# Optimization experiments

Hardware: AMD Instinct MI355X
Metric: run time of the kernel (lower is better)

## Reference

```python
import jax, jax.numpy as jnp
import numpy as np

HEADS = 16
HIDDEN = 1024
D_HEAD = HIDDEN // HEADS
SCALE = float(D_HEAD) ** 0.5


def setup_inputs() -> dict:
    key = jax.random.key(0)
    ks = jax.random.split(key, 11)
    B, L = 2, 2048
    x = jax.random.normal(ks[0], (B, L, HIDDEN), dtype=jnp.float32)
    # 0/1 padding mask, broadcast over heads and query positions
    mask = jax.random.randint(ks[1], (B, 1, 1, L), 0, 2).astype(jnp.float32)
    s = 1.0 / np.sqrt(HIDDEN)
    Wq = jax.random.normal(ks[2], (HIDDEN, HIDDEN), dtype=jnp.float32) * s
    bq = jax.random.normal(ks[3], (HIDDEN,), dtype=jnp.float32) * s
    Wk = jax.random.normal(ks[4], (HIDDEN, HIDDEN), dtype=jnp.float32) * s
    bk = jax.random.normal(ks[5], (HIDDEN,), dtype=jnp.float32) * s
    Wv = jax.random.normal(ks[6], (HIDDEN, HIDDEN), dtype=jnp.float32) * s
    bv = jax.random.normal(ks[7], (HIDDEN,), dtype=jnp.float32) * s
    Wo = jax.random.normal(ks[8], (HIDDEN, HIDDEN), dtype=jnp.float32) * s
    bo = jax.random.normal(ks[9], (HIDDEN,), dtype=jnp.float32) * s
    return {"x": x, "mask": mask, "Wq": Wq, "bq": bq, "Wk": Wk, "bk": bk,
            "Wv": Wv, "bv": bv, "Wo": Wo, "bo": bo}


def reference(x, mask, Wq, bq, Wk, bk, Wv, bv, Wo, bo):
    B, L, _ = x.shape
    # projections (Linear: x @ W + b), split heads -> [B, H, L, Dh]
    def proj(W, b):
        return (jnp.dot(x, W) + b).reshape(B, L, HEADS, D_HEAD).transpose(0, 2, 1, 3)
    q = proj(Wq, bq)
    k = proj(Wk, bk)
    v = proj(Wv, bv)
    # scaled dot-product with additive mask: scores [B, H, Lq, Lk]
    scores = jnp.einsum('bhqd,bhkd->bhqk', q, k) / SCALE + mask * (-10000.0)
    attn = jax.nn.softmax(scores, axis=-1)  # dropout p=0.0 -> identity
    out = jnp.einsum('bhqk,bhkd->bhqd', attn, v)
    out = out.transpose(0, 2, 1, 3).reshape(B, L, HIDDEN)
    return jnp.dot(out, Wo) + bo
```

## Files before the change

### kernel.cpp

```cpp
#include <hip/hip_runtime.h>
#include <math.h>

typedef unsigned short u16;
typedef short v8s __attribute__((ext_vector_type(8)));
typedef float v4f __attribute__((ext_vector_type(4)));
typedef float v16f __attribute__((ext_vector_type(16)));

#define HIDDEN 1024
#define L_SEQ 2048
#define NH 16
#define DH 64
#define NKMAX 1280

#define QSCALE 0.18033688011112042f

__device__ __forceinline__ u16 f2bf(float f) {
  union { float f; unsigned int i; } c; c.f = f;
  unsigned int x = c.i;
  unsigned int r = (x + 0x7fffu + ((x >> 16) & 1u)) >> 16;
  return (u16)r;
}

#if defined(__has_builtin)
#if __has_builtin(__builtin_amdgcn_cvt_pk_bf16_f32)
#define HAS_PKBF 1
#endif
#if __has_builtin(__builtin_amdgcn_exp2f)
#define EXP2(x) __builtin_amdgcn_exp2f(x)
#endif
#if __has_builtin(__builtin_amdgcn_rcpf)
#define RCP(x) __builtin_amdgcn_rcpf(x)
#endif
#endif
#ifndef EXP2
#define EXP2(x) exp2f(x)
#endif
#ifndef RCP
#define RCP(x) (1.0f / (x))
#endif

__device__ __forceinline__ unsigned pkbf(float a, float b) {
#ifdef HAS_PKBF
  typedef __bf16 v2bf __attribute__((ext_vector_type(2)));
  union { v2bf v; unsigned u; } c;
  c.v = __builtin_amdgcn_cvt_pk_bf16_f32(a, b);
  return c.u;
#else
  return (unsigned)f2bf(a) | ((unsigned)f2bf(b) << 16);
#endif
}

__device__ __forceinline__ void gload16(const void* g, void* l) {
  void* gg = const_cast<void*>(g);
  __builtin_amdgcn_global_load_lds(
      (__attribute__((address_space(1))) void*)gg,
      (__attribute__((address_space(3))) void*)l, 16, 0, 0);
}

__device__ __forceinline__ v16f vzero16() {
  v16f z;
#pragma unroll
  for (int i = 0; i < 16; ++i) z[i] = 0.f;
  return z;
}

__global__ __launch_bounds__(256) void prep(
    const float* __restrict__ x, u16* __restrict__ xb,
    const float* __restrict__ Wq, const float* __restrict__ Wk,
    const float* __restrict__ Wv, const float* __restrict__ Wo,
    u16* __restrict__ WtQ, u16* __restrict__ WtK,
    u16* __restrict__ WtV, u16* __restrict__ WtO,
    const float* __restrict__ maskg, u16* __restrict__ keep,
    unsigned* __restrict__ nkslot) {
  const int bid = blockIdx.x;
  const int t = threadIdx.x;

  if (bid < 2048) {
    const int i = (bid * 256 + t) * 8;
    const float4 a = *(const float4*)(x + i);
    const float4 b = *(const float4*)(x + i + 4);
    unsigned o[4] = {pkbf(a.x, a.y), pkbf(a.z, a.w), pkbf(b.x, b.y), pkbf(b.z, b.w)};
    *(uint4*)(xb + i) = *(const uint4*)o;
    return;
  }

  if (bid < 6144) {
    const int m = bid - 2048;
    const int z = m >> 10;
    const int rem = m & 1023;
    const int bx = rem & 31, by = rem >> 5;
    const float* src; u16* dst;
    if (z == 0) { src = Wq; dst = WtQ; }
    else if (z == 1) { src = Wk; dst = WtK; }
    else if (z == 2) { src = Wv; dst = WtV; }
    else { src = Wo; dst = WtO; }

    __shared__ u16 tile[32][33];
    const int tx = t & 31, ty = t >> 5;
    const int xcol = bx * 32 + tx;
    const int y0 = by * 32;
#pragma unroll
    for (int i = ty; i < 32; i += 8)
      tile[i][tx] = f2bf(src[(size_t)(y0 + i) * HIDDEN + xcol]);
    __syncthreads();
    const int xo = y0 + tx;
#pragma unroll
    for (int i = ty; i < 32; i += 8)
      dst[(size_t)(bx * 32 + i) * HIDDEN + xo] = tile[tx][i];
    return;
  }

  if (t < 64) {
    const int b = bid - 6144;
    const int lane = t;
    const float* mp = maskg + b * L_SEQ;
    int cnt = 0;
#pragma unroll 1
    for (int j = 0; j < 32; ++j) cnt += (mp[lane * 32 + j] == 0.0f) ? 1 : 0;
    int inc = cnt;
#pragma unroll
    for (int off = 1; off < 64; off <<= 1) {
      const int v = __shfl_up(inc, off, 64);
      if (lane >= off) inc += v;
    }
    int base = inc - cnt;
    u16* kp = keep + b * L_SEQ;
#pragma unroll 1
    for (int j = 0; j < 32; ++j) {
      const int k = lane * 32 + j;
      if (mp[k] == 0.0f) kp[base++] = (u16)k;
    }
    const int total = __shfl(inc, 63, 64);
    for (int i = total + lane; i < NKMAX; i += 64) kp[i] = 0;
    if (lane == 0) nkslot[b] = (unsigned)total;
  }
}

__global__ __launch_bounds__(256) void gemm128(
    const u16* __restrict__ A,
    const u16* __restrict__ B0, const u16* __restrict__ B1, const u16* __restrict__ B2,
    const float* __restrict__ bias0, const float* __restrict__ bias1, const float* __restrict__ bias2,
    u16* __restrict__ C0, u16* __restrict__ C1, u16* __restrict__ C2,
    float* __restrict__ Cf, const u16* __restrict__ keep,
    const unsigned* __restrict__ nkslot,
    int qkv_mode) {
  __shared__ __align__(16) u16 As[128 * 32];
  __shared__ __align__(16) u16 Bs[128 * 32];

  const u16* Bt; const float* bias; u16* C;
  if (blockIdx.z == 0) { Bt = B0; bias = bias0; C = C0; }
  else if (blockIdx.z == 1) { Bt = B1; bias = bias1; C = C1; }
  else { Bt = B2; bias = bias2; C = C2; }
  const int mode = qkv_mode ? (blockIdx.z == 0 ? 1 : (blockIdx.z == 1 ? 2 : 3)) : 0;
  const float oscale = (mode == 1) ? QSCALE : 1.0f;

  const int t = threadIdx.x;
  const int lane = t & 63;
  const int wave = t >> 6;
  const int quad = lane >> 4;
  const int l16 = lane & 15;
  const int wm = wave >> 1;
  const int wn = wave & 1;

  const int n0 = blockIdx.x * 128;
  const int sr = t >> 2;
  const int sc = (t & 3) * 8;

  int m0 = blockIdx.y * 128;
  int kvb = 0;
  const u16* Ag0;
  const u16* Ag1;
  if (mode == 2 || mode == 3) {
    const int y = blockIdx.y;
    if (y >= 20) return;
    kvb = y / 10;
    m0 = (y % 10) * 128;
    const unsigned nk = nkslot[kvb];
    if ((unsigned)m0 >= ((nk + 63u) & ~63u)) return;
    const int sr0 = keep[kvb * L_SEQ + m0 + sr];
    const int sr1 = keep[kvb * L_SEQ + m0 + 64 + sr];
    Ag0 = A + ((size_t)(kvb * L_SEQ + sr0)) * HIDDEN + sc;
    Ag1 = A + ((size_t)(kvb * L_SEQ + sr1)) * HIDDEN + sc;
  } else {
    Ag0 = A + (size_t)(m0 + sr) * HIDDEN + sc;
    Ag1 = Ag0 + (size_t)64 * HIDDEN;
  }
  const u16* Bg0 = Bt + (size_t)(n0 + sr) * HIDDEN + sc;
  const u16* Bg1 = Bg0 + (size_t)64 * HIDDEN;
  u16* Al0 = &As[sr * 32 + sc];
  u16* Al1 = &As[(64 + sr) * 32 + sc];
  u16* Bl0 = &Bs[sr * 32 + sc];
  u16* Bl1 = &Bs[(64 + sr) * 32 + sc];

  v4f acc[4][4];
#pragma unroll
  for (int mi = 0; mi < 4; ++mi)
#pragma unroll
    for (int ni = 0; ni < 4; ++ni)
      acc[mi][ni] = (v4f){0.f, 0.f, 0.f, 0.f};

  for (int k0 = 0; k0 < HIDDEN; k0 += 32) {
    __syncthreads();
    gload16(Ag0 + k0, Al0);
    gload16(Ag1 + k0, Al1);
    gload16(Bg0 + k0, Bl0);
    gload16(Bg1 + k0, Bl1);
    __syncthreads();

    v8s a[4], b[4];
#pragma unroll
    for (int mi = 0; mi < 4; ++mi)
      a[mi] = *(const v8s*)&As[(wm * 64 + mi * 16 + l16) * 32 + quad * 8];
#pragma unroll
    for (int ni = 0; ni < 4; ++ni)
      b[ni] = *(const v8s*)&Bs[(wn * 64 + ni * 16 + l16) * 32 + quad * 8];
#pragma unroll
    for (int mi = 0; mi < 4; ++mi)
#pragma unroll
      for (int ni = 0; ni < 4; ++ni)
        acc[mi][ni] = __builtin_amdgcn_mfma_f32_16x16x32_bf16(a[mi], b[ni], acc[mi][ni], 0, 0, 0);
  }

#pragma unroll
  for (int ni = 0; ni < 4; ++ni) {
    const int col = n0 + wn * 64 + ni * 16 + l16;
    const float bv = bias[col];
#pragma unroll
    for (int mi = 0; mi < 4; ++mi) {
      const int row0 = m0 + wm * 64 + mi * 16 + quad * 4;
      const float v0 = (acc[mi][ni][0] + bv) * oscale;
      const float v1 = (acc[mi][ni][1] + bv) * oscale;
      const float v2 = (acc[mi][ni][2] + bv) * oscale;
      const float v3 = (acc[mi][ni][3] + bv) * oscale;
      if (mode == 0) {
        Cf[(size_t)(row0 + 0) * HIDDEN + col] = v0;
        Cf[(size_t)(row0 + 1) * HIDDEN + col] = v1;
        Cf[(size_t)(row0 + 2) * HIDDEN + col] = v2;
        Cf[(size_t)(row0 + 3) * HIDDEN + col] = v3;
      } else if (mode == 1) {
        const int hh = col >> 6, d = col & 63;
        const float vv[4] = {v0, v1, v2, v3};
#pragma unroll
        for (int i = 0; i < 4; ++i) {
          const int rr = row0 + i;
          const int bb = rr >> 11, l = rr & 2047;
          C[((size_t)(bb * NH + hh) * L_SEQ + l) * DH + d] = f2bf(vv[i]);
        }
      } else if (mode == 2) {
        const int hh = col >> 6, d = col & 63;
        const float vv[4] = {v0, v1, v2, v3};
#pragma unroll
        for (int i = 0; i < 4; ++i)
          C[((size_t)(kvb * NH + hh) * L_SEQ + row0 + i) * DH + d] = f2bf(vv[i]);
      } else {
        const int hh = col >> 6, d = col & 63;
        unsigned pk[2] = {pkbf(v0, v1), pkbf(v2, v3)};
        *(uint2*)&C[((size_t)((kvb * NH + hh) * DH + d)) * L_SEQ + row0] = *(const uint2*)pk;
      }
    }
  }
}


#define XCH(D0_, D2_, A_, B_)                                        \
  {                                                                  \
    unsigned a_ = (A_), b_ = (B_);                                   \
    asm("v_permlane32_swap_b32 %0, %1" : "+v"(a_), "+v"(b_));        \
    D0_ = a_;                                      \
    D2_ = b_;                                      \
  }

#define MKPF(dst, P0, P1, P2, P3, P4, P5, P6, P7)                    \
  {                                                                  \
    const unsigned A_ = pkbf(P0, P1), C_ = pkbf(P2, P3);             \
    const unsigned B_ = pkbf(P4, P5), D_ = pkbf(P6, P7);             \
    union { unsigned u[4]; v8s v; } f_;                              \
    XCH(f_.u[0], f_.u[2], A_, B_);                                   \
    XCH(f_.u[1], f_.u[3], C_, D_);                                   \
    dst = f_.v;                                                      \
  }

__global__ __launch_bounds__(512) void attn512(
    const u16* __restrict__ Qg, const u16* __restrict__ Kcg, const u16* __restrict__ VTg,
    const unsigned* __restrict__ nkslot, u16* __restrict__ Og) {
  __shared__ __align__(16) u16 lds[32768];

  const int t = threadIdx.x;
  const int lane = t & 63;
  const int w = t >> 6;
  const int l31 = lane & 31;
  const int hi = lane >> 5;
  const int e7 = l31 & 7;

  const int bid = blockIdx.x;
  const int bh = bid & 31;
  const int q0 = (bid >> 5) * 256;
  const int b = bh >> 4;
  const int h = bh & 15;

  const size_t base = (size_t)bh * L_SEQ * DH;
  const u16* Qp = Qg + base;
  const u16* Kp = Kcg + base;
  const u16* VTp = VTg + base;

  const int nkb = (int)nkslot[b];
  const int ntiles = (nkb + 127) >> 7;

  const int r8 = lane >> 3, sl8 = lane & 7;
  const int koff = (w * 8 + r8) * DH + (sl8 ^ r8) * 8;
  const int r4 = lane >> 4, sl16 = lane & 15;
  const int vrow = w * 4 + r4;
  const int voff = vrow * L_SEQ + ((((sl16 & 7) ^ (vrow & 7)) | (sl16 & 8)) * 8);
  u16* const kd = &lds[(w * 8) * 64];
  u16* const vd = &lds[16384 + (w * 4) * 128];

  gload16(Kp + koff, kd);
  gload16(Kp + 64 * DH + koff, kd + 64 * 64);
  gload16(VTp + voff, vd);
  gload16(VTp + 32 * L_SEQ + voff, vd + 32 * 128);

  const int qrow = q0 + w * 32 + l31;
  v8s qf[4];
#pragma unroll
  for (int dc = 0; dc < 4; ++dc)
    qf[dc] = *(const v8s*)&Qp[(size_t)qrow * DH + dc * 16 + hi * 8];

  v16f oacc0 = vzero16(), oacc1 = vzero16();
  float lsum = 0.f;

  for (int n = 0; n < ntiles; ++n) {
    __syncthreads();
    const int ksb = (n & 1) * 8192;
    const int vtb = 16384 + (n & 1) * 8192;
    if (n + 1 < ntiles) {
      const size_t k1 = (size_t)(n + 1) * 128;
      const int s2 = ((n + 1) & 1) * 8192;
      gload16(Kp + k1 * DH + koff, kd + s2);
      gload16(Kp + (k1 + 64) * DH + koff, kd + s2 + 64 * 64);
      gload16(VTp + k1 + voff, vd + s2);
      gload16(VTp + k1 + 32 * L_SEQ + voff, vd + s2 + 32 * 128);
    }

    const int kb0 = n * 128;
#pragma unroll
    for (int hh = 0; hh < 2; ++hh) {
      const int h2 = hh ^ (w >> 2);
      v16f s0 = vzero16(), s1 = vzero16();
      __builtin_amdgcn_s_setprio(1);
#pragma unroll
      for (int dc = 0; dc < 4; ++dc) {
        const int po = ((dc * 2 + hi) ^ e7) * 8;
        const v8s kf0 = *(const v8s*)&lds[ksb + (h2 * 64 + l31) * 64 + po];
        const v8s kf1 = *(const v8s*)&lds[ksb + (h2 * 64 + 32 + l31) * 64 + po];
        s0 = __builtin_amdgcn_mfma_f32_32x32x16_bf16(kf0, qf[dc], s0, 0, 0, 0);
        s1 = __builtin_amdgcn_mfma_f32_32x32x16_bf16(kf1, qf[dc], s1, 0, 0, 0);
      }
      __builtin_amdgcn_s_setprio(0);

      const int kh0 = kb0 + h2 * 64;
      float p[32];
#pragma unroll
      for (int r = 0; r < 16; ++r) {
        p[r]      = EXP2(s0[r]);
        p[16 + r] = EXP2(s1[r]);
      }
      if (kh0 + 64 > nkb) {
#pragma unroll
        for (int r = 0; r < 16; ++r) {
          const int kk = kh0 + (r & 3) + 8 * (r >> 2) + 4 * hi;
          if (kk >= nkb) p[r] = 0.f;
          if (kk + 32 >= nkb) p[16 + r] = 0.f;
        }
      }
      {
        float a0 = 0.f, a1 = 0.f, a2 = 0.f, a3 = 0.f;
#pragma unroll
        for (int r = 0; r < 8; ++r) {
          a0 += p[r]; a1 += p[8 + r]; a2 += p[16 + r]; a3 += p[24 + r];
        }
        lsum += (a0 + a1) + (a2 + a3);
      }

      v8s pf0, pf1, pf2, pf3;
      MKPF(pf0, p[0],  p[1],  p[2],  p[3],  p[4],  p[5],  p[6],  p[7]);
      MKPF(pf1, p[8],  p[9],  p[10], p[11], p[12], p[13], p[14], p[15]);
      MKPF(pf2, p[16], p[17], p[18], p[19], p[20], p[21], p[22], p[23]);
      MKPF(pf3, p[24], p[25], p[26], p[27], p[28], p[29], p[30], p[31]);

      __builtin_amdgcn_s_setprio(1);
#pragma unroll
      for (int kc = 0; kc < 4; ++kc) {
        const v8s pb = (kc == 0) ? pf0 : (kc == 1) ? pf1 : (kc == 2) ? pf2 : pf3;
        const int oc = h2 * 8 + kc * 2 + hi;
        const int po = (((oc & 7) ^ e7) | (oc & 8)) * 8;
        const v8s vf0 = *(const v8s*)&lds[vtb + l31 * 128 + po];
        const v8s vf1 = *(const v8s*)&lds[vtb + (32 + l31) * 128 + po];
        oacc0 = __builtin_amdgcn_mfma_f32_32x32x16_bf16(vf0, pb, oacc0, 0, 0, 0);
        oacc1 = __builtin_amdgcn_mfma_f32_32x32x16_bf16(vf1, pb, oacc1, 0, 0, 0);
      }
      __builtin_amdgcn_s_setprio(0);
    }
  }

  const float ltot = lsum + __shfl(lsum, lane ^ 32, 64);
  const float linv = RCP(ltot);

  const size_t ob = ((size_t)(b * L_SEQ + qrow)) * HIDDEN + h * DH;
#pragma unroll
  for (int r = 0; r < 16; r += 2) {
    const int d0 = (r & 3) + 8 * (r >> 2) + 4 * hi;
    const unsigned w0 = pkbf(oacc0[r] * linv, oacc0[r + 1] * linv);
    const unsigned w1 = pkbf(oacc1[r] * linv, oacc1[r + 1] * linv);
    *(unsigned*)&Og[ob + d0] = w0;
    *(unsigned*)&Og[ob + 32 + d0] = w1;
  }
}

extern "C" void kernel_launch(void* const* d_in, const int* in_sizes, int n_in,
                              void* d_out, int out_size, void* d_ws, size_t ws_size,
                              hipStream_t stream) {
  const float* x    = (const float*)d_in[0];
  const float* mask = (const float*)d_in[1];
  const float* Wq   = (const float*)d_in[2];
  const float* bq   = (const float*)d_in[3];
  const float* Wk   = (const float*)d_in[4];
  const float* bk   = (const float*)d_in[5];
  const float* Wv   = (const float*)d_in[6];
  const float* bv   = (const float*)d_in[7];
  const float* Wo   = (const float*)d_in[8];
  const float* bo   = (const float*)d_in[9];
  float* out = (float*)d_out;
  u16* ws = (u16*)d_ws;

  const unsigned M1 = 1u << 20;
  u16* WtQ = ws;
  u16* WtK = ws + M1;
  u16* WtV = ws + 2 * M1;
  u16* WtO = ws + 3 * M1;
  u16* xb  = ws + 4 * M1;
  u16* Qb  = ws + 8 * M1;
  u16* Kc  = ws + 12 * M1;
  u16* VTc = ws + 16 * M1;
  u16* Ob  = ws + 20 * M1;
  u16* keep = ws + 16 * M1 - 8192;
  unsigned* nkslot = (unsigned*)(ws + 16 * M1 - 8192 - 8);

  prep<<<6146, 256, 0, stream>>>(x, xb, Wq, Wk, Wv, Wo, WtQ, WtK, WtV, WtO,
                                 mask, keep, nkslot);
  gemm128<<<dim3(8, 32, 3), 256, 0, stream>>>(xb, WtQ, WtK, WtV, bq, bk, bv,
                                              Qb, Kc, VTc, nullptr, keep, nkslot, 1);
  attn512<<<dim3(256), 512, 0, stream>>>(Qb, Kc, VTc, nkslot, Ob);
  gemm128<<<dim3(8, 32, 1), 256, 0, stream>>>(Ob, WtO, WtO, WtO, bo, bo, bo,
                                              nullptr, nullptr, nullptr, out, nullptr, nullptr, 0);
}
```

Before: 183.9 us.

## Deepen GEMM K-tile to 64 with XOR-swizzled LDS and XCD-aware block mapping

The projection GEMM now stages a 64-wide K slice per iteration instead of 32, which halves the number of barrier pairs and global-load rounds. The LDS layout is XOR-swizzled by row so the wider rows do not cause bank conflicts on the fragment reads. Launches switch to a 1D grid that is remapped so each XCD gets a contiguous band of M rows, aiming for better L2 reuse of A and B tiles. LDS use per block doubles, which may lower occupancy.

```diff
diff --git a/kernel.cpp b/kernel.cpp
--- a/kernel.cpp
+++ b/kernel.cpp
@@ -144,14 +144,22 @@
     float* __restrict__ Cf, const u16* __restrict__ keep,
     const unsigned* __restrict__ nkslot,
     int qkv_mode) {
-  __shared__ __align__(16) u16 As[128 * 32];
-  __shared__ __align__(16) u16 Bs[128 * 32];
+  __shared__ __align__(16) u16 As[128 * 64];
+  __shared__ __align__(16) u16 Bs[128 * 64];
+
+  const int wgid = blockIdx.x;
+  const int xcd = wgid & 7;
+  const int j = wgid >> 3;
+  const int bx = j & 7;
+  const int rem = j >> 3;
+  const int by = xcd * 4 + (rem & 3);
+  const int bz = rem >> 2;
 
   const u16* Bt; const float* bias; u16* C;
-  if (blockIdx.z == 0) { Bt = B0; bias = bias0; C = C0; }
-  else if (blockIdx.z == 1) { Bt = B1; bias = bias1; C = C1; }
+  if (bz == 0) { Bt = B0; bias = bias0; C = C0; }
+  else if (bz == 1) { Bt = B1; bias = bias1; C = C1; }
   else { Bt = B2; bias = bias2; C = C2; }
-  const int mode = qkv_mode ? (blockIdx.z == 0 ? 1 : (blockIdx.z == 1 ? 2 : 3)) : 0;
+  const int mode = qkv_mode ? (bz == 0 ? 1 : (bz == 1 ? 2 : 3)) : 0;
   const float oscale = (mode == 1) ? QSCALE : 1.0f;
 
   const int t = threadIdx.x;
@@ -162,35 +170,34 @@
   const int wm = wave >> 1;
   const int wn = wave & 1;
 
-  const int n0 = blockIdx.x * 128;
-  const int sr = t >> 2;
-  const int sc = (t & 3) * 8;
-
-  int m0 = blockIdx.y * 128;
+  const int n0 = bx * 128;
+
+  const int r0 = t >> 3;
+  const int og = ((t & 7) ^ (r0 & 7)) * 8;
+
+  int m0 = by * 128;
   int kvb = 0;
-  const u16* Ag0;
-  const u16* Ag1;
+  const u16* Ag[4];
   if (mode == 2 || mode == 3) {
-    const int y = blockIdx.y;
-    if (y >= 20) return;
-    kvb = y / 10;
-    m0 = (y % 10) * 128;
+    if (by >= 20) return;
+    kvb = by / 10;
+    m0 = (by % 10) * 128;
     const unsigned nk = nkslot[kvb];
     if ((unsigned)m0 >= ((nk + 63u) & ~63u)) return;
-    const int sr0 = keep[kvb * L_SEQ + m0 + sr];
-    const int sr1 = keep[kvb * L_SEQ + m0 + 64 + sr];
-    Ag0 = A + ((size_t)(kvb * L_SEQ + sr0)) * HIDDEN + sc;
-    Ag1 = A + ((size_t)(kvb * L_SEQ + sr1)) * HIDDEN + sc;
+#pragma unroll
+    for (int c = 0; c < 4; ++c) {
+      const int rr = keep[kvb * L_SEQ + m0 + r0 + 32 * c];
+      Ag[c] = A + ((size_t)(kvb * L_SEQ + rr)) * HIDDEN + og;
+    }
   } else {
-    Ag0 = A + (size_t)(m0 + sr) * HIDDEN + sc;
-    Ag1 = Ag0 + (size_t)64 * HIDDEN;
-  }
-  const u16* Bg0 = Bt + (size_t)(n0 + sr) * HIDDEN + sc;
-  const u16* Bg1 = Bg0 + (size_t)64 * HIDDEN;
-  u16* Al0 = &As[sr * 32 + sc];
-  u16* Al1 = &As[(64 + sr) * 32 + sc];
-  u16* Bl0 = &Bs[sr * 32 + sc];
-  u16* Bl1 = &Bs[(64 + sr) * 32 + sc];
+#pragma unroll
+    for (int c = 0; c < 4; ++c)
+      Ag[c] = A + (size_t)(m0 + r0 + 32 * c) * HIDDEN + og;
+  }
+  const u16* Bg0 = Bt + (size_t)(n0 + r0) * HIDDEN + og;
+
+  u16* const Ald = As + t * 8;
+  u16* const Bld = Bs + t * 8;
 
   v4f acc[4][4];
 #pragma unroll
@@ -199,26 +206,34 @@
     for (int ni = 0; ni < 4; ++ni)
       acc[mi][ni] = (v4f){0.f, 0.f, 0.f, 0.f};
 
-  for (int k0 = 0; k0 < HIDDEN; k0 += 32) {
+  for (int k0 = 0; k0 < HIDDEN; k0 += 64) {
     __syncthreads();
-    gload16(Ag0 + k0, Al0);
-    gload16(Ag1 + k0, Al1);
-    gload16(Bg0 + k0, Bl0);
-    gload16(Bg1 + k0, Bl1);
+#pragma unroll
+    for (int c = 0; c < 4; ++c) {
+      gload16(Ag[c] + k0, Ald + 2048 * c);
+      gload16(Bg0 + (size_t)(32 * c) * HIDDEN + k0, Bld + 2048 * c);
+    }
     __syncthreads();
 
-    v8s a[4], b[4];
-#pragma unroll
-    for (int mi = 0; mi < 4; ++mi)
-      a[mi] = *(const v8s*)&As[(wm * 64 + mi * 16 + l16) * 32 + quad * 8];
-#pragma unroll
-    for (int ni = 0; ni < 4; ++ni)
-      b[ni] = *(const v8s*)&Bs[(wn * 64 + ni * 16 + l16) * 32 + quad * 8];
-#pragma unroll
-    for (int mi = 0; mi < 4; ++mi)
-#pragma unroll
-      for (int ni = 0; ni < 4; ++ni)
-        acc[mi][ni] = __builtin_amdgcn_mfma_f32_16x16x32_bf16(a[mi], b[ni], acc[mi][ni], 0, 0, 0);
+#pragma unroll
+    for (int kk = 0; kk < 2; ++kk) {
+      v8s a[4], b[4];
+#pragma unroll
+      for (int mi = 0; mi < 4; ++mi) {
+        const int row = wm * 64 + mi * 16 + l16;
+        a[mi] = *(const v8s*)&As[row * 64 + (((kk * 4 + quad) ^ (row & 7)) * 8)];
+      }
+#pragma unroll
+      for (int ni = 0; ni < 4; ++ni) {
+        const int row = wn * 64 + ni * 16 + l16;
+        b[ni] = *(const v8s*)&Bs[row * 64 + (((kk * 4 + quad) ^ (row & 7)) * 8)];
+      }
+#pragma unroll
+      for (int mi = 0; mi < 4; ++mi)
+#pragma unroll
+        for (int ni = 0; ni < 4; ++ni)
+          acc[mi][ni] = __builtin_amdgcn_mfma_f32_16x16x32_bf16(a[mi], b[ni], acc[mi][ni], 0, 0, 0);
+    }
   }
 
 #pragma unroll
@@ -260,7 +275,6 @@
     }
   }
 }
-
 
 #define XCH(D0_, D2_, A_, B_)                                        \
   {                                                                  \
@@ -447,9 +461,9 @@
 
   prep<<<6146, 256, 0, stream>>>(x, xb, Wq, Wk, Wv, Wo, WtQ, WtK, WtV, WtO,
                                  mask, keep, nkslot);
-  gemm128<<<dim3(8, 32, 3), 256, 0, stream>>>(xb, WtQ, WtK, WtV, bq, bk, bv,
-                                              Qb, Kc, VTc, nullptr, keep, nkslot, 1);
+  gemm128<<<dim3(768), 256, 0, stream>>>(xb, WtQ, WtK, WtV, bq, bk, bv,
+                                         Qb, Kc, VTc, nullptr, keep, nkslot, 1);
   attn512<<<dim3(256), 512, 0, stream>>>(Qb, Kc, VTc, nkslot, Ob);
-  gemm128<<<dim3(8, 32, 1), 256, 0, stream>>>(Ob, WtO, WtO, WtO, bo, bo, bo,
-                                              nullptr, nullptr, nullptr, out, nullptr, nullptr, 0);
-}
+  gemm128<<<dim3(256), 256, 0, stream>>>(Ob, WtO, WtO, WtO, bo, bo, bo,
+                                         nullptr, nullptr, nullptr, out, nullptr, nullptr, 0);
+}
```

After: 187.5 us. Within noise of the previous version (+1.9%).
